# Optimization experiments

Measured on AMD Instinct MI355X. Metric: run time of the kernel, lower is better.

Reference implementation:

```python
import jax, jax.numpy as jnp
import numpy as np

B = 4
MAX_N = 2048
D = 512
H = 8
HD = D // H
SRC_LENS = [2048, 1536, 1800, 1200]   # sum = 6584
REF_LENS = [1900, 2048, 1400, 1600]   # sum = 6948
NEG_INF = -1e9


def setup_inputs() -> dict:
    key = jax.random.key(0)
    ks = jax.random.split(key, 8)
    n_src, n_ref = sum(SRC_LENS), sum(REF_LENS)
    s = 0.02
    return {
        "feats_src": jax.random.normal(ks[0], (n_src, D), dtype=jnp.float32),
        "batch_src": jnp.asarray(np.repeat(np.arange(B), SRC_LENS), dtype=jnp.int32),
        "feats_ref": jax.random.normal(ks[1], (n_ref, D), dtype=jnp.float32),
        "batch_ref": jnp.asarray(np.repeat(np.arange(B), REF_LENS), dtype=jnp.int32),
        "w_in": jax.random.normal(ks[2], (3 * D, D), dtype=jnp.float32) * s,
        "b_in": jnp.zeros((3 * D,), dtype=jnp.float32),
        "w_out": jax.random.normal(ks[3], (D, D), dtype=jnp.float32) * s,
        "b_out": jnp.zeros((D,), dtype=jnp.float32),
        "gw1": jax.random.normal(ks[4], (D, D), dtype=jnp.float32) * s,
        "gb1": jnp.zeros((D,), dtype=jnp.float32),
        "gw2": jax.random.normal(ks[5], (1, D), dtype=jnp.float32) * s,
        "gb2": jnp.zeros((1,), dtype=jnp.float32),
    }


def _to_dense(feats, batch_idx):
    # sparse [N, D] (sorted batch indices) -> dense [B, MAX_N, D] + key_padding_mask
    n = feats.shape[0]
    counts = jax.ops.segment_sum(jnp.ones((n,), jnp.int32), batch_idx, num_segments=B)
    starts = jnp.concatenate([jnp.zeros((1,), jnp.int32), jnp.cumsum(counts)[:-1].astype(jnp.int32)])
    pos = jnp.arange(n, dtype=jnp.int32) - starts[batch_idx]  # position within batch
    dense = jnp.zeros((B, MAX_N, feats.shape[1]), feats.dtype).at[batch_idx, pos].set(feats)
    mask = jnp.arange(MAX_N)[None, :] >= counts[:, None]  # True = padding (key_padding_mask)
    return dense, mask, pos


def reference(feats_src, batch_src, feats_ref, batch_ref,
              w_in, b_in, w_out, b_out, gw1, gb1, gw2, gb2):
    d_src, mask_src, pos_src = _to_dense(feats_src, batch_src)
    d_ref, mask_ref, _ = _to_dense(feats_ref, batch_ref)

    # nn.MultiheadAttention (batch_first, eval mode): packed in_proj, scaled dot-product
    q = (d_src @ w_in[:D].T + b_in[:D]).reshape(B, MAX_N, H, HD)
    k = (d_ref @ w_in[D:2 * D].T + b_in[D:2 * D]).reshape(B, MAX_N, H, HD)
    v = (d_ref @ w_in[2 * D:].T + b_in[2 * D:]).reshape(B, MAX_N, H, HD)
    scores = jnp.einsum('bqhd,bkhd->bhqk', q * (HD ** -0.5), k)
    scores = jnp.where(mask_ref[:, None, None, :], NEG_INF, scores)
    attn = jax.nn.softmax(scores, axis=-1)
    ctx = jnp.einsum('bhqk,bkhd->bqhd', attn, v).reshape(B, MAX_N, D)
    d_aligned = ctx @ w_out.T + b_out

    # gate MLP: Linear -> ReLU -> Linear -> Sigmoid
    gate = jax.nn.sigmoid(jax.nn.relu(d_aligned @ gw1.T + gb1) @ gw2.T + gb2)  # [B, MAX_N, 1]
    d_out = d_src + gate * d_aligned

    # dense -> ragged: gather each token back to its flat slot
    out_flat = d_out[batch_src, pos_src]  # [N_src, D]
    return out_flat, gate
```

## Files before the change

kernel.cpp:

```cpp
#include <hip/hip_runtime.h>
#include <hip/hip_bf16.h>


typedef __bf16 bf16x8_t __attribute__((ext_vector_type(8)));
typedef __bf16 bf16x4_t __attribute__((ext_vector_type(4)));
typedef float f32x4_t __attribute__((ext_vector_type(4)));
typedef float f32x2_t __attribute__((ext_vector_type(2)));

#define CQ_SCALE 0.18033688011112042f

__device__ inline bf16x8_t zero8() {
  bf16x8_t z;
#pragma unroll
  for (int t = 0; t < 8; ++t) z[t] = (__bf16)0.0f;
  return z;
}

__device__ __forceinline__ int sniff_f32(const void* w) {
  unsigned short u = ((const unsigned short*)w)[threadIdx.x & 63];
  return __ballot((u & 0x7F80) >= 0x3F80) != 0ULL;
}

__global__ void sentinel_k(float* out) {
  if (threadIdx.x == 0 && blockIdx.x == 0) out[0] = 1000.0f;
}

__global__ void cv_all(const void* w_in, const void* b_in, const void* w_out,
                       const void* b_out, const void* gw1, const void* gb1,
                       const void* gw2, const void* gb2,
                       __hip_bfloat16* __restrict__ ws) {
  int f = sniff_f32(w_in);
  const size_t F_W_IN = 16, F_B_IN = 786448, F_W_OUT = 787984, F_B_OUT = 1050128,
               F_GW1 = 1050640, F_GB1 = 1312784, F_GW2 = 1313296, F_GB2 = 1313808;
  const int total = 1313793;
  for (int g = blockIdx.x * 256 + threadIdx.x; g < total; g += gridDim.x * 256) {
    const void* src;
    size_t dst;
    int i;
    if (g < 786432) { src = w_in; dst = F_W_IN; i = g; }
    else if (g < 787968) { src = b_in; dst = F_B_IN; i = g - 786432; }
    else if (g < 1050112) { src = w_out; dst = F_W_OUT; i = g - 787968; }
    else if (g < 1050624) { src = b_out; dst = F_B_OUT; i = g - 1050112; }
    else if (g < 1312768) { src = gw1; dst = F_GW1; i = g - 1050624; }
    else if (g < 1313280) { src = gb1; dst = F_GB1; i = g - 1312768; }
    else if (g < 1313792) { src = gw2; dst = F_GW2; i = g - 1313280; }
    else { src = gb2; dst = F_GB2; i = g - 1313792; }
    ws[dst + i] = f ? __float2bfloat16(((const float*)src)[i])
                    : ((const __hip_bfloat16*)src)[i];
  }
}

__device__ __forceinline__ void gemm_core(
    const void* __restrict__ A_, long aoff, const __hip_bfloat16* __restrict__ Bt,
    const __hip_bfloat16* __restrict__ bias, __hip_bfloat16* __restrict__ C,
    int M, int K, int lda, int ldc, float cscale, int relu, int f, int bm, int bn,
    __bf16 (&As)[128][64], __bf16 (&Bs)[128][64]) {
  int tid = threadIdx.x, lane = tid & 63, wave = tid >> 6;
  int wm = wave >> 1, wn = wave & 1;
  int l15 = lane & 15, quad = lane >> 4;

  f32x4_t acc[4][4];
#pragma unroll
  for (int i = 0; i < 4; ++i)
#pragma unroll
    for (int j = 0; j < 4; ++j)
#pragma unroll
      for (int r = 0; r < 4; ++r) acc[i][j][r] = 0.f;

  bf16x8_t ra[4], rb[4];
  f32x4_t raf[4][2];

  auto gload = [&](int k0) {
#pragma unroll
    for (int s = 0; s < 4; ++s) {
      int id = s * 256 + tid;
      int row = id >> 3, col = (id & 7) * 8;
      int arow = bm + row;
      if (f) {
        if (arow < M) {
          const float* p = (const float*)A_ + aoff + (size_t)arow * lda + k0 + col;
          raf[s][0] = *reinterpret_cast<const f32x4_t*>(p);
          raf[s][1] = *reinterpret_cast<const f32x4_t*>(p + 4);
        } else {
#pragma unroll
          for (int e = 0; e < 4; ++e) { raf[s][0][e] = 0.f; raf[s][1][e] = 0.f; }
        }
      } else {
        ra[s] = (arow < M)
                    ? *reinterpret_cast<const bf16x8_t*>((const __hip_bfloat16*)A_ + aoff +
                                                         (size_t)arow * lda + k0 + col)
                    : zero8();
      }
      rb[s] = *reinterpret_cast<const bf16x8_t*>(Bt + (size_t)(bn + row) * 512 + k0 + col);
    }
  };
  auto stage = [&]() {
#pragma unroll
    for (int s = 0; s < 4; ++s) {
      int id = s * 256 + tid;
      int row = id >> 3, col = (id & 7) * 8;
      if (f) {
        bf16x8_t t;
#pragma unroll
        for (int e = 0; e < 4; ++e) {
          t[e] = (__bf16)raf[s][0][e];
          t[4 + e] = (__bf16)raf[s][1][e];
        }
        *reinterpret_cast<bf16x8_t*>(&As[row][col]) = t;
      } else {
        *reinterpret_cast<bf16x8_t*>(&As[row][col]) = ra[s];
      }
      *reinterpret_cast<bf16x8_t*>(&Bs[row][col]) = rb[s];
    }
  };

  int nk = K >> 6;
  gload(0);
  for (int it = 0; it < nk; ++it) {
    stage();
    __syncthreads();
    if (it + 1 < nk) gload((it + 1) * 64);
#pragma unroll
    for (int ks = 0; ks < 2; ++ks) {
      bf16x8_t af[4], bfv[4];
#pragma unroll
      for (int i = 0; i < 4; ++i)
        af[i] = *reinterpret_cast<const bf16x8_t*>(
            &As[wm * 64 + i * 16 + l15][ks * 32 + quad * 8]);
#pragma unroll
      for (int j = 0; j < 4; ++j)
        bfv[j] = *reinterpret_cast<const bf16x8_t*>(
            &Bs[wn * 64 + j * 16 + l15][ks * 32 + quad * 8]);
#pragma unroll
      for (int i = 0; i < 4; ++i)
#pragma unroll
        for (int j = 0; j < 4; ++j)
          acc[i][j] = __builtin_amdgcn_mfma_f32_16x16x32_bf16(af[i], bfv[j], acc[i][j], 0, 0, 0);
    }
    __syncthreads();
  }

#pragma unroll
  for (int i = 0; i < 4; ++i)
#pragma unroll
    for (int j = 0; j < 4; ++j) {
      int col = bn + wn * 64 + j * 16 + l15;
      float bv = __bfloat162float(bias[col]);
#pragma unroll
      for (int r = 0; r < 4; ++r) {
        int row = bm + wm * 64 + i * 16 + quad * 4 + r;
        if (row < M) {
          float v = (acc[i][j][r] + bv) * cscale;
          if (relu) v = fmaxf(v, 0.f);
          C[(size_t)row * ldc + col] = __float2bfloat16(v);
        }
      }
    }
}

__global__ __launch_bounds__(256) void proj2(
    const void* __restrict__ fs, const void* __restrict__ fr,
    const __hip_bfloat16* __restrict__ ws, __hip_bfloat16* __restrict__ Q,
    __hip_bfloat16* __restrict__ KV, const void* snf) {
  __shared__ __bf16 As[128][64];
  __shared__ __bf16 Bs[128][64];
  const size_t F_W_IN = 16, F_B_IN = 786448;
  int f = sniff_f32(snf);
  int bid = blockIdx.x;
  if (bid < 208) {
    int bx = bid >> 2, by = bid & 3;
    gemm_core(fs, 0, ws + F_W_IN, ws + F_B_IN, Q, 6584, 512, 512, 512, CQ_SCALE, 0, f,
              bx * 128, by * 128, As, Bs);
  } else {
    int k = bid - 208;
    int bx = k >> 3, by = k & 7;
    gemm_core(fr, 0, ws + F_W_IN + 262144, ws + F_B_IN + 512, KV, 6948, 512, 512, 1024,
              1.0f, 0, f, bx * 128, by * 128, As, Bs);
  }
}

template <bool AF32>
__global__ __launch_bounds__(256) void gemm128(
    const void* __restrict__ A_, long aoff, const __hip_bfloat16* __restrict__ Bt,
    const __hip_bfloat16* __restrict__ bias, __hip_bfloat16* __restrict__ C,
    int M, int K, int lda, int ldc, float cscale, int relu, const void* snf) {
  __shared__ __bf16 As[128][64];
  __shared__ __bf16 Bs[128][64];
  int f = 0;
  if constexpr (AF32) f = sniff_f32(snf);
  gemm_core(A_, aoff, Bt, bias, C, M, K, lda, ldc, cscale, relu, f,
            blockIdx.x * 128, blockIdx.y * 128, As, Bs);
}

__global__ __launch_bounds__(256) void gemm128_pv(
    const __hip_bfloat16* __restrict__ P0, const __hip_bfloat16* __restrict__ P1,
    const float* __restrict__ L, const __hip_bfloat16* __restrict__ Bt,
    const __hip_bfloat16* __restrict__ bias, __hip_bfloat16* __restrict__ C,
    int M) {
  __shared__ __bf16 As[128][64];
  __shared__ __bf16 Bs[128][64];
  int tid = threadIdx.x, lane = tid & 63, wave = tid >> 6;
  int wm = wave >> 1, wn = wave & 1;
  int l15 = lane & 15, quad = lane >> 4;
  int bm = blockIdx.x * 128, bn = blockIdx.y * 128;

  f32x4_t acc[4][4];
#pragma unroll
  for (int i = 0; i < 4; ++i)
#pragma unroll
    for (int j = 0; j < 4; ++j)
#pragma unroll
      for (int r = 0; r < 4; ++r) acc[i][j][r] = 0.f;

  bf16x8_t rp0[4], rp1[4], rb[4];
  f32x2_t rl[4];

  auto gload = [&](int k0) {
    int h = k0 >> 6;
#pragma unroll
    for (int s = 0; s < 4; ++s) {
      int id = s * 256 + tid;
      int row = id >> 3, col = (id & 7) * 8;
      int arow = bm + row;
      if (arow < M) {
        size_t off = (size_t)arow * 512 + k0 + col;
        rp0[s] = *reinterpret_cast<const bf16x8_t*>(P0 + off);
        rp1[s] = *reinterpret_cast<const bf16x8_t*>(P1 + off);
        rl[s] = *reinterpret_cast<const f32x2_t*>(&L[((size_t)arow * 8 + h) * 2]);
      } else {
        rp0[s] = zero8();
        rp1[s] = zero8();
        rl[s][0] = 1.f;
        rl[s][1] = 0.f;
      }
      rb[s] = *reinterpret_cast<const bf16x8_t*>(Bt + (size_t)(bn + row) * 512 + k0 + col);
    }
  };
  auto stage = [&]() {
#pragma unroll
    for (int s = 0; s < 4; ++s) {
      int id = s * 256 + tid;
      int row = id >> 3, col = (id & 7) * 8;
      float sc = 1.0f / (rl[s][0] + rl[s][1]);
      float w0 = rl[s][0] * sc, w1 = rl[s][1] * sc;
      bf16x8_t t;
#pragma unroll
      for (int e = 0; e < 8; ++e)
        t[e] = (__bf16)(w0 * (float)rp0[s][e] + w1 * (float)rp1[s][e]);
      *reinterpret_cast<bf16x8_t*>(&As[row][col]) = t;
      *reinterpret_cast<bf16x8_t*>(&Bs[row][col]) = rb[s];
    }
  };

  gload(0);
  for (int it = 0; it < 8; ++it) {
    stage();
    __syncthreads();
    if (it + 1 < 8) gload((it + 1) * 64);
#pragma unroll
    for (int ks = 0; ks < 2; ++ks) {
      bf16x8_t af[4], bfv[4];
#pragma unroll
      for (int i = 0; i < 4; ++i)
        af[i] = *reinterpret_cast<const bf16x8_t*>(
            &As[wm * 64 + i * 16 + l15][ks * 32 + quad * 8]);
#pragma unroll
      for (int j = 0; j < 4; ++j)
        bfv[j] = *reinterpret_cast<const bf16x8_t*>(
            &Bs[wn * 64 + j * 16 + l15][ks * 32 + quad * 8]);
#pragma unroll
      for (int i = 0; i < 4; ++i)
#pragma unroll
        for (int j = 0; j < 4; ++j)
          acc[i][j] = __builtin_amdgcn_mfma_f32_16x16x32_bf16(af[i], bfv[j], acc[i][j], 0, 0, 0);
    }
    __syncthreads();
  }

#pragma unroll
  for (int i = 0; i < 4; ++i)
#pragma unroll
    for (int j = 0; j < 4; ++j) {
      int col = bn + wn * 64 + j * 16 + l15;
      float bv = __bfloat162float(bias[col]);
#pragma unroll
      for (int r = 0; r < 4; ++r) {
        int row = bm + wm * 64 + i * 16 + quad * 4 + r;
        if (row < M)
          C[(size_t)row * 512 + col] = __float2bfloat16(acc[i][j][r] + bv);
      }
    }
}

__device__ __forceinline__ void flash_core(
    const __hip_bfloat16* __restrict__ Qb, const __hip_bfloat16* __restrict__ KVb,
    __hip_bfloat16* __restrict__ OUTb, float* __restrict__ LPb, int nsrc, int nref,
    int qt, int kt0, int ktNfull, int do_tail,
    __bf16 (&VtL)[2][64][72], __bf16 (&PL)[4][32][72]) {
  int h = blockIdx.y;
  int tid = threadIdx.x, lane = tid & 63, wave = tid >> 6;
  int l15 = lane & 15, quad = lane >> 4;
  int Mb = nsrc + 1;
  int qbase = qt * 128 + wave * 32;

  bf16x8_t qfr[2][2];
#pragma unroll
  for (int g = 0; g < 2; ++g) {
    int qrow = qbase + g * 16 + l15;
#pragma unroll
    for (int ks = 0; ks < 2; ++ks)
      qfr[g][ks] = (qrow < nsrc)
                       ? *reinterpret_cast<const bf16x8_t*>(
                             Qb + (size_t)qrow * 512 + h * 64 + ks * 32 + quad * 8)
                       : zero8();
  }

  f32x4_t O[2][4];
#pragma unroll
  for (int g = 0; g < 2; ++g)
#pragma unroll
    for (int j = 0; j < 4; ++j)
#pragma unroll
      for (int r = 0; r < 4; ++r) O[g][j][r] = 0.f;
  float lsum[2] = {0.f, 0.f};

  bf16x8_t kf[8], v0, v1;
  auto loadK = [&](int k0) {
#pragma unroll
    for (int j = 0; j < 4; ++j) {
      const __hip_bfloat16* kp =
          KVb + (size_t)(k0 + j * 16 + l15) * 1024 + h * 64 + quad * 8;
      kf[j * 2] = *reinterpret_cast<const bf16x8_t*>(kp);
      kf[j * 2 + 1] = *reinterpret_cast<const bf16x8_t*>(kp + 32);
    }
  };
  auto loadV = [&](int k0) {
    const __hip_bfloat16* vp = KVb + (size_t)(k0 + lane) * 1024 + 512 + h * 64 + wave * 16;
    v0 = *reinterpret_cast<const bf16x8_t*>(vp);
    v1 = *reinterpret_cast<const bf16x8_t*>(vp + 8);
  };

  int nit = ktNfull - kt0;
  if (nit > 0) {
    loadK(kt0 * 64);
    loadV(kt0 * 64);
  }

  for (int it = 0; it < nit; ++it) {
    int k0 = (kt0 + it) * 64;
    __bf16(*Vt)[72] = VtL[it & 1];
#pragma unroll
    for (int e = 0; e < 8; ++e) {
      Vt[wave * 16 + e][lane] = v0[e];
      Vt[wave * 16 + 8 + e][lane] = v1[e];
    }
    if (it + 1 < nit) loadV(k0 + 64);

    f32x4_t St[2][4];
#pragma unroll
    for (int g = 0; g < 2; ++g)
#pragma unroll
      for (int j = 0; j < 4; ++j)
#pragma unroll
        for (int r = 0; r < 4; ++r) St[g][j][r] = 0.f;
#pragma unroll
    for (int g = 0; g < 2; ++g)
#pragma unroll
      for (int j = 0; j < 4; ++j)
#pragma unroll
        for (int ks = 0; ks < 2; ++ks)
          St[g][j] = __builtin_amdgcn_mfma_f32_16x16x32_bf16(kf[j * 2 + ks], qfr[g][ks],
                                                             St[g][j], 0, 0, 0);
    if (it + 1 < nit) loadK(k0 + 64);

#pragma unroll
    for (int g = 0; g < 2; ++g)
#pragma unroll
      for (int j = 0; j < 4; ++j) {
        bf16x4_t pk;
#pragma unroll
        for (int r = 0; r < 4; ++r) {
          float p = exp2f(St[g][j][r]);
          lsum[g] += p;
          pk[r] = (__bf16)p;
        }
        *reinterpret_cast<bf16x4_t*>(&PL[wave][g * 16 + l15][j * 16 + quad * 4]) = pk;
      }

    __syncthreads();

    bf16x8_t pa[2][2];
#pragma unroll
    for (int g = 0; g < 2; ++g)
#pragma unroll
      for (int ks = 0; ks < 2; ++ks)
        pa[g][ks] = *reinterpret_cast<const bf16x8_t*>(
            &PL[wave][g * 16 + l15][ks * 32 + quad * 8]);
#pragma unroll
    for (int j = 0; j < 4; ++j)
#pragma unroll
      for (int ks = 0; ks < 2; ++ks) {
        bf16x8_t vbf =
            *reinterpret_cast<const bf16x8_t*>(&Vt[j * 16 + l15][ks * 32 + quad * 8]);
#pragma unroll
        for (int g = 0; g < 2; ++g)
          O[g][j] = __builtin_amdgcn_mfma_f32_16x16x32_bf16(pa[g][ks], vbf, O[g][j], 0, 0, 0);
      }
  }

  if (do_tail) {
    int k0 = ktNfull * 64;
    __bf16(*Vt)[72] = VtL[nit & 1];
    {
      int kr = k0 + lane;
      const __hip_bfloat16* vp = KVb + (size_t)kr * 1024 + 512 + h * 64 + wave * 16;
      bf16x8_t t0 = (kr < nref) ? *reinterpret_cast<const bf16x8_t*>(vp) : zero8();
      bf16x8_t t1 = (kr < nref) ? *reinterpret_cast<const bf16x8_t*>(vp + 8) : zero8();
#pragma unroll
      for (int e = 0; e < 8; ++e) {
        Vt[wave * 16 + e][lane] = t0[e];
        Vt[wave * 16 + 8 + e][lane] = t1[e];
      }
    }
#pragma unroll
    for (int j = 0; j < 4; ++j) {
      int kcol = k0 + j * 16 + l15;
      const __hip_bfloat16* kp = KVb + (size_t)kcol * 1024 + h * 64 + quad * 8;
      kf[j * 2] = (kcol < nref) ? *reinterpret_cast<const bf16x8_t*>(kp) : zero8();
      kf[j * 2 + 1] = (kcol < nref) ? *reinterpret_cast<const bf16x8_t*>(kp + 32) : zero8();
    }
#pragma unroll
    for (int g = 0; g < 2; ++g) {
      f32x4_t St[4];
#pragma unroll
      for (int j = 0; j < 4; ++j)
#pragma unroll
        for (int r = 0; r < 4; ++r) St[j][r] = 0.f;
#pragma unroll
      for (int j = 0; j < 4; ++j)
#pragma unroll
        for (int ks = 0; ks < 2; ++ks)
          St[j] = __builtin_amdgcn_mfma_f32_16x16x32_bf16(kf[j * 2 + ks], qfr[g][ks],
                                                          St[j], 0, 0, 0);
#pragma unroll
      for (int j = 0; j < 4; ++j) {
        bf16x4_t pk;
#pragma unroll
        for (int r = 0; r < 4; ++r) {
          int kl = k0 + j * 16 + quad * 4 + r;
          float p = (kl < nref) ? exp2f(St[j][r]) : 0.f;
          lsum[g] += p;
          pk[r] = (__bf16)p;
        }
        *reinterpret_cast<bf16x4_t*>(&PL[wave][g * 16 + l15][j * 16 + quad * 4]) = pk;
      }
    }
    __syncthreads();
    bf16x8_t pa[2][2];
#pragma unroll
    for (int g = 0; g < 2; ++g)
#pragma unroll
      for (int ks = 0; ks < 2; ++ks)
        pa[g][ks] = *reinterpret_cast<const bf16x8_t*>(
            &PL[wave][g * 16 + l15][ks * 32 + quad * 8]);
#pragma unroll
    for (int j = 0; j < 4; ++j)
#pragma unroll
      for (int ks = 0; ks < 2; ++ks) {
        bf16x8_t vbf =
            *reinterpret_cast<const bf16x8_t*>(&Vt[j * 16 + l15][ks * 32 + quad * 8]);
#pragma unroll
        for (int g = 0; g < 2; ++g)
          O[g][j] = __builtin_amdgcn_mfma_f32_16x16x32_bf16(pa[g][ks], vbf, O[g][j], 0, 0, 0);
      }
  }

#pragma unroll
  for (int g = 0; g < 2; ++g) {
    lsum[g] += __shfl_xor(lsum[g], 16);
    lsum[g] += __shfl_xor(lsum[g], 32);
  }

  if (LPb && quad == 0) {
#pragma unroll
    for (int g = 0; g < 2; ++g) {
      int row = qbase + g * 16 + l15;
      if (row < Mb) LPb[((size_t)row * 8 + h) * 2] = lsum[g];
    }
  }

#pragma unroll
  for (int g = 0; g < 2; ++g)
#pragma unroll
    for (int r = 0; r < 4; ++r) {
      int row = qbase + g * 16 + quad * 4 + r;
      if (row < Mb) {
        float li = __shfl(lsum[g], quad * 4 + r);
        float inv = 1.0f / li;
#pragma unroll
        for (int j = 0; j < 4; ++j)
          OUTb[(size_t)row * 512 + h * 64 + j * 16 + l15] =
              __float2bfloat16(O[g][j][r] * inv);
      }
    }
}

__global__ __launch_bounds__(256) void flash_all(
    const __hip_bfloat16* __restrict__ Q, const __hip_bfloat16* __restrict__ KV,
    __hip_bfloat16* __restrict__ O0, __hip_bfloat16* __restrict__ O1,
    float* __restrict__ L, int nsplit) {
  const int TILE_START[4] = {0, 17, 30, 45};
  const int SRC_START[4] = {0, 2048, 3584, 5384};
  const int REF_START[4] = {0, 1900, 3948, 5348};
  const int SRC_LEN[4] = {2048, 1536, 1800, 1200};
  const int REF_LEN[4] = {1900, 2048, 1400, 1600};
  const int CS[4] = {0, 2049, 3586, 5387};
  __shared__ __bf16 VtL[2][64][72];
  __shared__ __bf16 PL[4][32][72];
  int bid = blockIdx.x;
  int b = (bid >= TILE_START[3]) ? 3 : (bid >= TILE_START[2]) ? 2 : (bid >= TILE_START[1]) ? 1 : 0;
  int qt = bid - TILE_START[b];
  int nref = REF_LEN[b];
  int full = nref >> 6, nkt = (nref + 63) >> 6, rem = nref & 63;
  int split = blockIdx.z;
  int kt0, ktN, tail;
  if (nsplit == 1) { kt0 = 0; ktN = full; tail = rem > 0; }
  else if (split == 0) { int half = nkt >> 1; kt0 = 0; ktN = half; tail = 0; }
  else { int half = nkt >> 1; kt0 = half; ktN = full; tail = rem > 0; }
  __hip_bfloat16* OUT = (nsplit == 1 || split == 0) ? O0 : O1;
  float* LP = (nsplit == 1) ? nullptr : (L + split + (size_t)CS[b] * 16);
  flash_core(Q + (size_t)SRC_START[b] * 512, KV + (size_t)REF_START[b] * 1024,
             OUT + (size_t)CS[b] * 512, LP, SRC_LEN[b], nref, qt, kt0, ktN, tail, VtL, PL);
}

__global__ __launch_bounds__(256) void flash_one(const __hip_bfloat16* __restrict__ Qb,
                                                 const __hip_bfloat16* __restrict__ KVb,
                                                 __hip_bfloat16* __restrict__ OUTb,
                                                 int nsrc, int nref) {
  __shared__ __bf16 VtL[2][64][72];
  __shared__ __bf16 PL[4][32][72];
  flash_core(Qb, KVb, OUTb, nullptr, nsrc, nref, blockIdx.x, 0, nref >> 6,
             (nref & 63) > 0, VtL, PL);
}

__global__ __launch_bounds__(256) void finalize_all(
    const void* __restrict__ src, const __hip_bfloat16* __restrict__ aligned,
    const __hip_bfloat16* __restrict__ hidden, const __hip_bfloat16* __restrict__ gw2,
    const __hip_bfloat16* __restrict__ gb2, void* __restrict__ out, const void* snf) {
  int f = sniff_f32(snf);
  int lane = threadIdx.x & 63;
  int r = blockIdx.x * 4 + (threadIdx.x >> 6);
  int b = (r >= 5387) ? 3 : (r >= 3586) ? 2 : (r >= 2049) ? 1 : 0;
  const int CS[4] = {0, 2049, 3586, 5387};
  const int NSRC[4] = {2048, 1536, 1800, 1200};
  int pos = r - CS[b];

  float zacc = 0.f;
  const __hip_bfloat16* hrow = hidden + (size_t)r * 512;
#pragma unroll
  for (int t = 0; t < 8; ++t) {
    int c = lane + (t << 6);
    zacc += __bfloat162float(hrow[c]) * __bfloat162float(gw2[c]);
  }
  for (int o = 32; o; o >>= 1) zacc += __shfl_xor(zacc, o);
  zacc += __bfloat162float(gb2[0]);
  float g = 1.f / (1.f + __expf(-zacc));

  const size_t GOFF = (size_t)6584 * 512;
  if (pos < NSRC[b]) {
    size_t ib = (size_t)(r - b) * 512;
    const __hip_bfloat16* arow = aligned + (size_t)r * 512;
#pragma unroll
    for (int t = 0; t < 8; ++t) {
      int c = lane + (t << 6);
      float sv = f ? ((const float*)src)[ib + c]
                   : __bfloat162float(((const __hip_bfloat16*)src)[ib + c]);
      float val = sv + g * __bfloat162float(arow[c]);
      if (f) ((float*)out)[ib + c] = val;
      else ((__hip_bfloat16*)out)[ib + c] = __float2bfloat16(val);
    }
    if (lane == 0) {
      size_t go = GOFF + b * 2048 + pos;
      if (f) ((float*)out)[go] = g;
      else ((__hip_bfloat16*)out)[go] = __float2bfloat16(g);
    }
  } else {
    for (int p = NSRC[b] + lane; p < 2048; p += 64) {
      size_t go = GOFF + b * 2048 + p;
      if (f) ((float*)out)[go] = g;
      else ((__hip_bfloat16*)out)[go] = __float2bfloat16(g);
    }
  }
}

__global__ __launch_bounds__(256) void finalize_b(
    const void* __restrict__ src, const __hip_bfloat16* __restrict__ alnb,
    const __hip_bfloat16* __restrict__ hidb, const __hip_bfloat16* __restrict__ gw2,
    const __hip_bfloat16* __restrict__ gb2, void* __restrict__ out,
    int b, int nsrc, int src_start, const void* snf) {
  int f = sniff_f32(snf);
  int lane = threadIdx.x & 63;
  int r = blockIdx.x * 4 + (threadIdx.x >> 6);
  if (r > nsrc) return;

  float zacc = 0.f;
  const __hip_bfloat16* hrow = hidb + (size_t)r * 512;
#pragma unroll
  for (int t = 0; t < 8; ++t) {
    int c = lane + (t << 6);
    zacc += __bfloat162float(hrow[c]) * __bfloat162float(gw2[c]);
  }
  for (int o = 32; o; o >>= 1) zacc += __shfl_xor(zacc, o);
  zacc += __bfloat162float(gb2[0]);
  float g = 1.f / (1.f + __expf(-zacc));

  const size_t GOFF = (size_t)6584 * 512;
  if (r < nsrc) {
    size_t ib = (size_t)(src_start + r) * 512;
    const __hip_bfloat16* arow = alnb + (size_t)r * 512;
#pragma unroll
    for (int t = 0; t < 8; ++t) {
      int c = lane + (t << 6);
      float sv = f ? ((const float*)src)[ib + c]
                   : __bfloat162float(((const __hip_bfloat16*)src)[ib + c]);
      float val = sv + g * __bfloat162float(arow[c]);
      if (f) ((float*)out)[ib + c] = val;
      else ((__hip_bfloat16*)out)[ib + c] = __float2bfloat16(val);
    }
    if (lane == 0) {
      size_t go = GOFF + b * 2048 + r;
      if (f) ((float*)out)[go] = g;
      else ((__hip_bfloat16*)out)[go] = __float2bfloat16(g);
    }
  } else {
    for (int p = nsrc + lane; p < 2048; p += 64) {
      size_t go = GOFF + b * 2048 + p;
      if (f) ((float*)out)[go] = g;
      else ((__hip_bfloat16*)out)[go] = __float2bfloat16(g);
    }
  }
}

extern "C" void kernel_launch(void* const* d_in, const int* in_sizes, int n_in,
                              void* d_out, int out_size, void* d_ws, size_t ws_size,
                              hipStream_t stream) {
  (void)in_sizes; (void)n_in; (void)out_size;
  const void* feats_src = d_in[0];
  const void* feats_ref = d_in[2];
  const void* w_in = d_in[4];
  const void* b_in = d_in[5];
  const void* w_out = d_in[6];
  const void* b_out = d_in[7];
  const void* gw1 = d_in[8];
  const void* gb1 = d_in[9];
  const void* gw2 = d_in[10];
  const void* gb2 = d_in[11];

  const size_t F_W_IN = 16, F_B_IN = 786448, F_W_OUT = 787984, F_B_OUT = 1050128,
               F_GW1 = 1050640, F_GB1 = 1312784, F_GW2 = 1313296, F_GB2 = 1313808,
               A0 = 1313824;
  const size_t NEED_A2 = 2 * 22139936;
  const size_t NEED_A = 2 * 15178784;
  const size_t NEED_B = 2 * (A0 + 4259840);

  if (ws_size < NEED_B) {
    sentinel_k<<<1, 64, 0, stream>>>((float*)d_out);
    return;
  }

  __hip_bfloat16* ws = (__hip_bfloat16*)d_ws;
  cv_all<<<dim3(1024), dim3(256), 0, stream>>>(w_in, b_in, w_out, b_out, gw1, gb1, gw2,
                                               gb2, ws);

  const int SRC_LEN[4] = {2048, 1536, 1800, 1200};
  const int REF_LEN[4] = {1900, 2048, 1400, 1600};
  const int SRC_START[4] = {0, 2048, 3584, 5384};
  const int REF_START[4] = {0, 1900, 3948, 5348};
  dim3 blk(256);

  if (ws_size >= NEED_A) {
    __hip_bfloat16* R1 = ws + A0;
    __hip_bfloat16* R2 = R1 + 3375104;
    __hip_bfloat16* R3 = R2 + 7114752;
    proj2<<<dim3(648), blk, 0, stream>>>(feats_src, feats_ref, ws, R1, R2, w_in);
    if (ws_size >= NEED_A2) {
      __hip_bfloat16* P0 = R3 + 3375104;
      __hip_bfloat16* P1 = P0 + 3375104;
      float* L = (float*)(ws + 21928992);
      flash_all<<<dim3(55, 8, 2), blk, 0, stream>>>(R1, R2, P0, P1, L, 2);
      gemm128_pv<<<dim3(52, 4), blk, 0, stream>>>(P0, P1, L, ws + F_W_OUT, ws + F_B_OUT,
                                                  R1, 6588);
    } else {
      flash_all<<<dim3(55, 8, 1), blk, 0, stream>>>(R1, R2, R3, nullptr, nullptr, 1);
      gemm128<false><<<dim3(52, 4), blk, 0, stream>>>(R3, 0, ws + F_W_OUT, ws + F_B_OUT,
                                                      R1, 6588, 512, 512, 512, 1.0f, 0,
                                                      nullptr);
    }
    gemm128<false><<<dim3(52, 4), blk, 0, stream>>>(R1, 0, ws + F_GW1, ws + F_GB1, R3,
                                                    6588, 512, 512, 512, 1.0f, 1,
                                                    nullptr);
    finalize_all<<<dim3(1647), blk, 0, stream>>>(feats_src, R1, R3, ws + F_GW2,
                                                 ws + F_GB2, d_out, w_in);
  } else {
    __hip_bfloat16* W2 = ws + A0;
    __hip_bfloat16* W1 = W2 + 2097152;
    __hip_bfloat16* W3 = W1 + 1081344;
    for (int b = 0; b < 4; ++b) {
      int nsrc = SRC_LEN[b], nref = REF_LEN[b];
      gemm128<true><<<dim3((nsrc + 127) / 128, 4), blk, 0, stream>>>(
          feats_src, (long)SRC_START[b] * 512, ws + F_W_IN, ws + F_B_IN, W1, nsrc, 512,
          512, 512, CQ_SCALE, 0, w_in);
      gemm128<true><<<dim3((nref + 127) / 128, 8), blk, 0, stream>>>(
          feats_ref, (long)REF_START[b] * 512, ws + F_W_IN + 262144, ws + F_B_IN + 512,
          W2, nref, 512, 512, 1024, 1.0f, 0, w_in);
      flash_one<<<dim3((nsrc + 128) / 128, 8), blk, 0, stream>>>(W1, W2, W3, nsrc, nref);
      gemm128<false><<<dim3((nsrc + 128) / 128, 4), blk, 0, stream>>>(
          W3, 0, ws + F_W_OUT, ws + F_B_OUT, W1, nsrc + 1, 512, 512, 512, 1.0f, 0,
          nullptr);
      gemm128<false><<<dim3((nsrc + 128) / 128, 4), blk, 0, stream>>>(
          W1, 0, ws + F_GW1, ws + F_GB1, W3, nsrc + 1, 512, 512, 512, 1.0f, 1, nullptr);
      finalize_b<<<dim3((nsrc + 4) / 4), blk, 0, stream>>>(
          feats_src, W1, W3, ws + F_GW2, ws + F_GB2, d_out, b, nsrc, SRC_START[b], w_in);
    }
  }
}
```

Measured before the change: 250.7 us.

## Fuse gate MLP GEMM with sigmoid and residual finalize into one kernel

Replaces the separate gate hidden-layer GEMM and the finalize kernel with a single kernel that computes the gw1 GEMM per 64-row tile, applies ReLU and the gw2 dot product in registers, then writes the gated residual output. This removes the round trip of the hidden activation through global memory and one launch. In exchange it launches only about a hundred blocks that each walk all output columns serially, which lowers parallelism. The flash split logic is also generalized to an arbitrary split count with a single strided partial buffer.

New measurement: 324.6 us. 1.29x slower.

```diff
diff --git a/kernel.cpp b/kernel.cpp
--- a/kernel.cpp
+++ b/kernel.cpp
@@ -294,8 +294,8 @@
 
 __device__ __forceinline__ void flash_core(
     const __hip_bfloat16* __restrict__ Qb, const __hip_bfloat16* __restrict__ KVb,
-    __hip_bfloat16* __restrict__ OUTb, float* __restrict__ LPb, int nsrc, int nref,
-    int qt, int kt0, int ktNfull, int do_tail,
+    __hip_bfloat16* __restrict__ OUTb, float* __restrict__ LPb, int lstride,
+    int nsrc, int nref, int qt, int kt0, int ktNfull, int do_tail,
     __bf16 (&VtL)[2][64][72], __bf16 (&PL)[4][32][72]) {
   int h = blockIdx.y;
   int tid = threadIdx.x, lane = tid & 63, wave = tid >> 6;
@@ -485,7 +485,7 @@
 #pragma unroll
     for (int g = 0; g < 2; ++g) {
       int row = qbase + g * 16 + l15;
-      if (row < Mb) LPb[((size_t)row * 8 + h) * 2] = lsum[g];
+      if (row < Mb) LPb[((size_t)row * 8 + h) * lstride] = lsum[g];
     }
   }
 
@@ -507,8 +507,7 @@
 
 __global__ __launch_bounds__(256) void flash_all(
     const __hip_bfloat16* __restrict__ Q, const __hip_bfloat16* __restrict__ KV,
-    __hip_bfloat16* __restrict__ O0, __hip_bfloat16* __restrict__ O1,
-    float* __restrict__ L, int nsplit) {
+    __hip_bfloat16* __restrict__ P, long pstride, float* __restrict__ L, int nsplit) {
   const int TILE_START[4] = {0, 17, 30, 45};
   const int SRC_START[4] = {0, 2048, 3584, 5384};
   const int REF_START[4] = {0, 1900, 3948, 5348};
@@ -521,16 +520,17 @@
   int b = (bid >= TILE_START[3]) ? 3 : (bid >= TILE_START[2]) ? 2 : (bid >= TILE_START[1]) ? 1 : 0;
   int qt = bid - TILE_START[b];
   int nref = REF_LEN[b];
-  int full = nref >> 6, nkt = (nref + 63) >> 6, rem = nref & 63;
+  int full = nref >> 6, rem = nref & 63, nkt = full + (rem > 0);
   int split = blockIdx.z;
-  int kt0, ktN, tail;
-  if (nsplit == 1) { kt0 = 0; ktN = full; tail = rem > 0; }
-  else if (split == 0) { int half = nkt >> 1; kt0 = 0; ktN = half; tail = 0; }
-  else { int half = nkt >> 1; kt0 = half; ktN = full; tail = rem > 0; }
-  __hip_bfloat16* OUT = (nsplit == 1 || split == 0) ? O0 : O1;
-  float* LP = (nsplit == 1) ? nullptr : (L + split + (size_t)CS[b] * 16);
+  int kt0 = nkt * split / nsplit;
+  int ktEnd = nkt * (split + 1) / nsplit;
+  int ktNfull = (ktEnd < full) ? ktEnd : full;
+  int tail = (ktEnd == nkt && rem > 0) ? 1 : 0;
+  __hip_bfloat16* OUT = P + (size_t)split * pstride;
+  float* LP = (nsplit == 1) ? nullptr : (L + split + (size_t)CS[b] * 8 * nsplit);
   flash_core(Q + (size_t)SRC_START[b] * 512, KV + (size_t)REF_START[b] * 1024,
-             OUT + (size_t)CS[b] * 512, LP, SRC_LEN[b], nref, qt, kt0, ktN, tail, VtL, PL);
+             OUT + (size_t)CS[b] * 512, LP, nsplit, SRC_LEN[b], nref, qt, kt0, ktNfull,
+             tail, VtL, PL);
 }
 
 __global__ __launch_bounds__(256) void flash_one(const __hip_bfloat16* __restrict__ Qb,
@@ -539,56 +539,137 @@
                                                  int nsrc, int nref) {
   __shared__ __bf16 VtL[2][64][72];
   __shared__ __bf16 PL[4][32][72];
-  flash_core(Qb, KVb, OUTb, nullptr, nsrc, nref, blockIdx.x, 0, nref >> 6,
+  flash_core(Qb, KVb, OUTb, nullptr, 1, nsrc, nref, blockIdx.x, 0, nref >> 6,
              (nref & 63) > 0, VtL, PL);
 }
 
-__global__ __launch_bounds__(256) void finalize_all(
-    const void* __restrict__ src, const __hip_bfloat16* __restrict__ aligned,
-    const __hip_bfloat16* __restrict__ hidden, const __hip_bfloat16* __restrict__ gw2,
-    const __hip_bfloat16* __restrict__ gb2, void* __restrict__ out, const void* snf) {
-  int f = sniff_f32(snf);
-  int lane = threadIdx.x & 63;
-  int r = blockIdx.x * 4 + (threadIdx.x >> 6);
-  int b = (r >= 5387) ? 3 : (r >= 3586) ? 2 : (r >= 2049) ? 1 : 0;
+__global__ __launch_bounds__(256) void gate_fin(
+    const void* __restrict__ src, const __hip_bfloat16* __restrict__ ALN,
+    const __hip_bfloat16* __restrict__ gw1b, const __hip_bfloat16* __restrict__ gb1b,
+    const __hip_bfloat16* __restrict__ gw2b, const __hip_bfloat16* __restrict__ gb2b,
+    void* __restrict__ out, const void* snf) {
+  __shared__ __bf16 As[64][64];
+  __shared__ __bf16 Bs[128][64];
   const int CS[4] = {0, 2049, 3586, 5387};
   const int NSRC[4] = {2048, 1536, 1800, 1200};
-  int pos = r - CS[b];
-
-  float zacc = 0.f;
-  const __hip_bfloat16* hrow = hidden + (size_t)r * 512;
-#pragma unroll
-  for (int t = 0; t < 8; ++t) {
-    int c = lane + (t << 6);
-    zacc += __bfloat162float(hrow[c]) * __bfloat162float(gw2[c]);
-  }
-  for (int o = 32; o; o >>= 1) zacc += __shfl_xor(zacc, o);
-  zacc += __bfloat162float(gb2[0]);
-  float g = 1.f / (1.f + __expf(-zacc));
+  int f = sniff_f32(snf);
+  int tid = threadIdx.x, lane = tid & 63, w = tid >> 6;
+  int l15 = lane & 15, quad = lane >> 4;
+  int bm = blockIdx.x * 64;
+
+  float gacc[4] = {0.f, 0.f, 0.f, 0.f};
+  bf16x8_t ra[2], rb[4];
+
+  for (int ct = 0; ct < 4; ++ct) {
+    int bnn = ct * 128;
+    f32x4_t acc[8];
+#pragma unroll
+    for (int j = 0; j < 8; ++j)
+#pragma unroll
+      for (int r = 0; r < 4; ++r) acc[j][r] = 0.f;
+
+    auto gload = [&](int k0) {
+#pragma unroll
+      for (int s = 0; s < 2; ++s) {
+        int id = s * 256 + tid;
+        int row = id >> 3, col = (id & 7) * 8;
+        int arow = bm + row;
+        ra[s] = (arow < 6588)
+                    ? *reinterpret_cast<const bf16x8_t*>(ALN + (size_t)arow * 512 + k0 + col)
+                    : zero8();
+      }
+#pragma unroll
+      for (int s = 0; s < 4; ++s) {
+        int id = s * 256 + tid;
+        int row = id >> 3, col = (id & 7) * 8;
+        rb[s] = *reinterpret_cast<const bf16x8_t*>(gw1b + (size_t)(bnn + row) * 512 + k0 + col);
+      }
+    };
+    auto stage = [&]() {
+#pragma unroll
+      for (int s = 0; s < 2; ++s) {
+        int id = s * 256 + tid;
+        *reinterpret_cast<bf16x8_t*>(&As[id >> 3][(id & 7) * 8]) = ra[s];
+      }
+#pragma unroll
+      for (int s = 0; s < 4; ++s) {
+        int id = s * 256 + tid;
+        *reinterpret_cast<bf16x8_t*>(&Bs[id >> 3][(id & 7) * 8]) = rb[s];
+      }
+    };
+
+    gload(0);
+    for (int it = 0; it < 8; ++it) {
+      stage();
+      __syncthreads();
+      if (it + 1 < 8) gload((it + 1) * 64);
+#pragma unroll
+      for (int ks = 0; ks < 2; ++ks) {
+        bf16x8_t af = *reinterpret_cast<const bf16x8_t*>(
+            &As[w * 16 + l15][ks * 32 + quad * 8]);
+#pragma unroll
+        for (int j = 0; j < 8; ++j) {
+          bf16x8_t bv = *reinterpret_cast<const bf16x8_t*>(
+              &Bs[j * 16 + l15][ks * 32 + quad * 8]);
+          acc[j] = __builtin_amdgcn_mfma_f32_16x16x32_bf16(af, bv, acc[j], 0, 0, 0);
+        }
+      }
+      __syncthreads();
+    }
+
+#pragma unroll
+    for (int j = 0; j < 8; ++j) {
+      int col = bnn + j * 16 + l15;
+      float b1 = __bfloat162float(gb1b[col]);
+      float w2 = __bfloat162float(gw2b[col]);
+#pragma unroll
+      for (int r = 0; r < 4; ++r) gacc[r] += fmaxf(acc[j][r] + b1, 0.f) * w2;
+    }
+  }
+
+#pragma unroll
+  for (int r = 0; r < 4; ++r) {
+    gacc[r] += __shfl_xor(gacc[r], 1);
+    gacc[r] += __shfl_xor(gacc[r], 2);
+    gacc[r] += __shfl_xor(gacc[r], 4);
+    gacc[r] += __shfl_xor(gacc[r], 8);
+  }
+  float gb2v = __bfloat162float(gb2b[0]);
+  float gv[4];
+#pragma unroll
+  for (int r = 0; r < 4; ++r) gv[r] = 1.f / (1.f + __expf(-(gacc[r] + gb2v)));
 
   const size_t GOFF = (size_t)6584 * 512;
-  if (pos < NSRC[b]) {
-    size_t ib = (size_t)(r - b) * 512;
-    const __hip_bfloat16* arow = aligned + (size_t)r * 512;
-#pragma unroll
-    for (int t = 0; t < 8; ++t) {
-      int c = lane + (t << 6);
-      float sv = f ? ((const float*)src)[ib + c]
-                   : __bfloat162float(((const __hip_bfloat16*)src)[ib + c]);
-      float val = sv + g * __bfloat162float(arow[c]);
-      if (f) ((float*)out)[ib + c] = val;
-      else ((__hip_bfloat16*)out)[ib + c] = __float2bfloat16(val);
-    }
-    if (lane == 0) {
-      size_t go = GOFF + b * 2048 + pos;
-      if (f) ((float*)out)[go] = g;
-      else ((__hip_bfloat16*)out)[go] = __float2bfloat16(g);
-    }
-  } else {
-    for (int p = NSRC[b] + lane; p < 2048; p += 64) {
-      size_t go = GOFF + b * 2048 + p;
-      if (f) ((float*)out)[go] = g;
-      else ((__hip_bfloat16*)out)[go] = __float2bfloat16(g);
+#pragma unroll
+  for (int rr = 0; rr < 16; ++rr) {
+    int row = bm + w * 16 + rr;
+    if (row >= 6588) continue;
+    float g = __shfl(gv[rr & 3], (rr >> 2) * 16);
+    int b = (row >= 5387) ? 3 : (row >= 3586) ? 2 : (row >= 2049) ? 1 : 0;
+    int pos = row - CS[b];
+    if (pos < NSRC[b]) {
+      size_t ib = (size_t)(row - b) * 512;
+      const __hip_bfloat16* arow = ALN + (size_t)row * 512;
+#pragma unroll
+      for (int t = 0; t < 8; ++t) {
+        int c = lane + (t << 6);
+        float sv = f ? ((const float*)src)[ib + c]
+                     : __bfloat162float(((const __hip_bfloat16*)src)[ib + c]);
+        float val = sv + g * __bfloat162float(arow[c]);
+        if (f) ((float*)out)[ib + c] = val;
+        else ((__hip_bfloat16*)out)[ib + c] = __float2bfloat16(val);
+      }
+      if (lane == 0) {
+        size_t go = GOFF + b * 2048 + pos;
+        if (f) ((float*)out)[go] = g;
+        else ((__hip_bfloat16*)out)[go] = __float2bfloat16(g);
+      }
+    } else {
+      for (int p = NSRC[b] + lane; p < 2048; p += 64) {
+        size_t go = GOFF + b * 2048 + p;
+        if (f) ((float*)out)[go] = g;
+        else ((__hip_bfloat16*)out)[go] = __float2bfloat16(g);
+      }
     }
   }
 }
@@ -659,6 +740,9 @@
   const size_t F_W_IN = 16, F_B_IN = 786448, F_W_OUT = 787984, F_B_OUT = 1050128,
                F_GW1 = 1050640, F_GB1 = 1312784, F_GW2 = 1313296, F_GB2 = 1313808,
                A0 = 1313824;
+  const size_t OFF_P = 15178784;
+  const size_t PSTRIDE = 3375104;
+  const size_t OFF_L2 = 21928992;
   const size_t NEED_A2 = 2 * 22139936;
   const size_t NEED_A = 2 * 15178784;
   const size_t NEED_B = 2 * (A0 + 4259840);
@@ -684,23 +768,19 @@
     __hip_bfloat16* R3 = R2 + 7114752;
     proj2<<<dim3(648), blk, 0, stream>>>(feats_src, feats_ref, ws, R1, R2, w_in);
     if (ws_size >= NEED_A2) {
-      __hip_bfloat16* P0 = R3 + 3375104;
-      __hip_bfloat16* P1 = P0 + 3375104;
-      float* L = (float*)(ws + 21928992);
-      flash_all<<<dim3(55, 8, 2), blk, 0, stream>>>(R1, R2, P0, P1, L, 2);
-      gemm128_pv<<<dim3(52, 4), blk, 0, stream>>>(P0, P1, L, ws + F_W_OUT, ws + F_B_OUT,
-                                                  R1, 6588);
+      __hip_bfloat16* P = ws + OFF_P;
+      float* L = (float*)(ws + OFF_L2);
+      flash_all<<<dim3(55, 8, 2), blk, 0, stream>>>(R1, R2, P, PSTRIDE, L, 2);
+      gemm128_pv<<<dim3(52, 4), blk, 0, stream>>>(P, P + PSTRIDE, L, ws + F_W_OUT,
+                                                  ws + F_B_OUT, R1, 6588);
     } else {
-      flash_all<<<dim3(55, 8, 1), blk, 0, stream>>>(R1, R2, R3, nullptr, nullptr, 1);
+      flash_all<<<dim3(55, 8, 1), blk, 0, stream>>>(R1, R2, R3, 0, nullptr, 1);
       gemm128<false><<<dim3(52, 4), blk, 0, stream>>>(R3, 0, ws + F_W_OUT, ws + F_B_OUT,
                                                       R1, 6588, 512, 512, 512, 1.0f, 0,
                                                       nullptr);
     }
-    gemm128<false><<<dim3(52, 4), blk, 0, stream>>>(R1, 0, ws + F_GW1, ws + F_GB1, R3,
-                                                    6588, 512, 512, 512, 1.0f, 1,
-                                                    nullptr);
-    finalize_all<<<dim3(1647), blk, 0, stream>>>(feats_src, R1, R3, ws + F_GW2,
-                                                 ws + F_GB2, d_out, w_in);
+    gate_fin<<<dim3(103), blk, 0, stream>>>(feats_src, R1, ws + F_GW1, ws + F_GB1,
+                                            ws + F_GW2, ws + F_GB2, d_out, w_in);
   } else {
     __hip_bfloat16* W2 = ws + A0;
     __hip_bfloat16* W1 = W2 + 2097152;
```
